# Optimization experiments

Measured on AMD Instinct MI355X. Metric: run time of the kernel, lower is better.

Reference implementation:

```python
import jax, jax.numpy as jnp
import numpy as np

NUM_HEADS = 12
HEAD_DIM = 64
HIDDEN = NUM_HEADS * HEAD_DIM  # 768


def setup_inputs() -> dict:
    key = jax.random.key(0)
    ks = jax.random.split(key, 18)
    B, Ni, Nt, H = 8, 1024, 512, HIDDEN
    inp = {
        "hidden_states": jax.random.normal(ks[0], (B, Ni, H), jnp.float32),
        "text": jax.random.normal(ks[1], (B, Nt, H), jnp.float32),
    }
    names = ["Wq", "Wk", "Wv", "Wqt", "Wkt", "Wvt", "Wo"]
    for i, n in enumerate(names):
        inp[n] = jax.random.normal(ks[2 + i], (H, H), jnp.float32) * 0.02
        inp["b" + n[1:]] = jnp.zeros((H,), jnp.float32)
    return inp


def _split_heads(x):
    # [B, S, H] -> [B, h, S, dh]
    B, S, _ = x.shape
    return x.reshape(B, S, NUM_HEADS, HEAD_DIM).transpose(0, 2, 1, 3)


def _merge_heads(x):
    # [B, h, S, dh] -> [B, S, H]
    B, h, S, dh = x.shape
    return x.transpose(0, 2, 1, 3).reshape(B, S, h * dh)


def _attend(q, k, v):
    scale = 1.0 / jnp.sqrt(jnp.asarray(HEAD_DIM, q.dtype))
    scores = jnp.einsum("bhqd,bhkd->bhqk", q, k) * scale
    probs = jax.nn.softmax(scores, axis=-1)
    ctx = jnp.einsum("bhqk,bhkd->bhqd", probs, v)
    return ctx, probs


def reference(hidden_states, text, Wq, bq, Wk, bk, Wv, bv,
              Wqt, bqt, Wkt, bkt, Wvt, bvt, Wo, bo):
    q_i = _split_heads(hidden_states @ Wq + bq)
    k_i = _split_heads(hidden_states @ Wk + bk)
    v_i = _split_heads(hidden_states @ Wv + bv)
    q_t = _split_heads(text @ Wqt + bqt)
    k_t = _split_heads(text @ Wkt + bkt)
    v_t = _split_heads(text @ Wvt + bvt)

    ctx_ii, weights = _attend(q_i, k_i, v_i)   # img -> img (weights returned, vis=True)
    ctx_tt, _ = _attend(q_t, k_t, v_t)         # text -> text
    ctx_it, _ = _attend(q_i, k_t, v_t)         # img queries, text keys/values
    ctx_ti, _ = _attend(q_t, k_i, v_i)         # text queries, img keys/values

    out_img = (_merge_heads(ctx_ii) + _merge_heads(ctx_it)) * 0.5 @ Wo + bo
    out_text = (_merge_heads(ctx_tt) + _merge_heads(ctx_ti)) * 0.5 @ Wo + bo
    return out_img, out_text, weights
```

## Files before the change

### kernel.cpp

```cpp
#include <hip/hip_runtime.h>

typedef __attribute__((ext_vector_type(4))) float f32x4;
typedef __attribute__((ext_vector_type(8))) short short8;
typedef __attribute__((ext_vector_type(4))) short s16x4;
typedef __attribute__((ext_vector_type(4))) unsigned short us4;
typedef unsigned short u16;
typedef unsigned char uchar;

__device__ __forceinline__ u16 f2b(float f) {
  union { float f; unsigned u; } a; a.f = f;
  unsigned r = a.u + 0x7fffu + ((a.u >> 16) & 1u);
  return (u16)(r >> 16);
}
__device__ __forceinline__ unsigned cvtpk2(float lo, float hi) {
  unsigned r;
  asm("v_cvt_pk_bf16_f32 %0, %1, %2" : "=v"(r) : "v"(lo), "v"(hi));
  return r;
}
__device__ __forceinline__ short8 cvt8(f32x4 a, f32x4 b) {
  union { unsigned u[4]; short8 s; } r;
  r.u[0] = cvtpk2(a[0], a[1]); r.u[1] = cvtpk2(a[2], a[3]);
  r.u[2] = cvtpk2(b[0], b[1]); r.u[3] = cvtpk2(b[2], b[3]);
  return r.s;
}
#define SWZ(r, byteoff) ((((r) * 128) + (byteoff)) ^ (((r) & 7) << 4))
#define C2 0.18033688011112158f

typedef __attribute__((address_space(1))) const void* gp1;
typedef __attribute__((address_space(3))) void* lp3;
__device__ __forceinline__ void gload16(const void* g, void* lds_wave_uniform_base) {
  __builtin_amdgcn_global_load_lds((gp1)g, (lp3)lds_wave_uniform_base, 16, 0, 0);
}
__device__ __forceinline__ void waitv0() { asm volatile("s_waitcnt vmcnt(0)" ::: "memory"); }
__device__ __forceinline__ void waitv1() { asm volatile("s_waitcnt vmcnt(1)" ::: "memory"); }
__device__ __forceinline__ void waitv2() { asm volatile("s_waitcnt vmcnt(2)" ::: "memory"); }
__device__ __forceinline__ void abar()  { __builtin_amdgcn_s_barrier(); }
__device__ __forceinline__ void sbar()  { __builtin_amdgcn_sched_barrier(0); }

__global__ __launch_bounds__(256) void prep_kernel(
    const float* w0, const float* w1, const float* w2, const float* w3,
    const float* w4, const float* w5, const float* w6, u16* wt,
    const float* __restrict__ h, const float* __restrict__ tx, u16* __restrict__ xb)
{
  const int bid = blockIdx.x, t = threadIdx.x;
  if (bid < 1008) {
    __shared__ float tile[64][65];
    const float* Ws[7] = {w0, w1, w2, w3, w4, w5, w6};
    int z = bid / 144, rem = bid % 144;
    const float* W = Ws[z];
    u16* out = wt + (size_t)z * 589824;
    const int r0 = (rem / 12) * 64, c0 = (rem % 12) * 64;
#pragma unroll
    for (int i = 0; i < 4; ++i) {
      int idx = i * 256 + t;
      int r = idx >> 4, c = (idx & 15) * 4;
      f32x4 v = *(const f32x4*)(W + (size_t)(r0 + r) * 768 + (c0 + c));
      tile[r][c + 0] = v[0]; tile[r][c + 1] = v[1];
      tile[r][c + 2] = v[2]; tile[r][c + 3] = v[3];
    }
    __syncthreads();
#pragma unroll
    for (int i = 0; i < 4; ++i) {
      int idx = i * 256 + t;
      int rn = idx >> 4, c = (idx & 15) * 4;
      union { us4 o; unsigned u[2]; } o;
      o.u[0] = cvtpk2(tile[c + 0][rn], tile[c + 1][rn]);
      o.u[1] = cvtpk2(tile[c + 2][rn], tile[c + 3][rn]);
      *(us4*)(out + (size_t)(c0 + rn) * 768 + (r0 + c)) = o.o;
    }
  } else {
    size_t e = ((size_t)(bid - 1008) * 256 + t) * 8;
    const float* src; size_t off;
    if (e < 6291456) { src = h; off = e; } else { src = tx; off = e - 6291456; }
    f32x4 v0 = *(const f32x4*)(src + off), v1 = *(const f32x4*)(src + off + 4);
    *(short8*)(xb + e) = cvt8(v0, v1);
  }
}

__global__ __launch_bounds__(256) void proj_kernel(
    const u16* __restrict__ Xb, const u16* __restrict__ wt,
    const float* __restrict__ bq, const float* __restrict__ bk, const float* __restrict__ bv,
    const float* __restrict__ bqt, const float* __restrict__ bkt, const float* __restrict__ bvt,
    u16* __restrict__ qi, u16* __restrict__ ki, u16* __restrict__ vti,
    u16* __restrict__ qt, u16* __restrict__ ktx, u16* __restrict__ vtt)
{
  const int bid = blockIdx.x;
  const int wk = (bid & 7) * 216 + (bid >> 3);
  const bool img = wk < 1152;
  const int id = img ? wk : wk - 1152;
  const int sg = id / 72, r72 = id % 72;
  const int y = r72 >> 2;
  const int x = sg * 4 + (r72 & 3);
  const int z = y / 6, n0 = (y % 6) * 128, m0 = x * 128;
  const int S = img ? 1024 : 512, logS = img ? 10 : 9;
  const u16* X = img ? Xb : Xb + 6291456;
  const u16* Wt = wt + (img ? 0 : (size_t)3 * 589824) + (size_t)y * 98304;
  const float* bias = img ? (z == 0 ? bq : z == 1 ? bk : bv)
                          : (z == 0 ? bqt : z == 1 ? bkt : bvt);
  u16* out = img ? (z == 0 ? qi : z == 1 ? ki : vti)
                 : (z == 0 ? qt : z == 1 ? ktx : vtt);
  const bool vmode = (z == 2);
  __shared__ unsigned char sm[36864];
  unsigned char* Asm = sm;
  unsigned char* Bsm = sm + 16384;
  const int t = threadIdx.x, w = t >> 6, l = t & 63;
  const int wm = (w & 1) * 64, wn = (w >> 1) * 64;
  f32x4 acc[4][4] = {};
  for (int k0 = 0; k0 < 768; k0 += 64) {
#pragma unroll
    for (int j = 0; j < 4; ++j) {
      int chunk = j * 4 + w;
      int r = chunk * 8 + (l >> 3);
      int cb = ((l & 7) * 16) ^ ((r & 7) << 4);
      gload16(X + (size_t)(m0 + r) * 768 + k0 + cb / 2, Asm + chunk * 1024);
    }
#pragma unroll
    for (int j = 0; j < 4; ++j) {
      int chunk = j * 4 + w;
      int r = chunk * 8 + (l >> 3);
      int cb = ((l & 7) * 16) ^ ((r & 7) << 4);
      gload16(Wt + (size_t)r * 768 + k0 + cb / 2, Bsm + chunk * 1024);
    }
    __syncthreads();
#pragma unroll
    for (int kc = 0; kc < 2; ++kc) {
      short8 af[4], bfr[4];
      const int koff = (kc * 32 + (l >> 4) * 8) * 2;
#pragma unroll
      for (int ms = 0; ms < 4; ++ms) {
        int row = wm + ms * 16 + (l & 15);
        af[ms] = *(const short8*)(Asm + SWZ(row, koff));
      }
#pragma unroll
      for (int ns = 0; ns < 4; ++ns) {
        int row = wn + ns * 16 + (l & 15);
        bfr[ns] = *(const short8*)(Bsm + SWZ(row, koff));
      }
      __builtin_amdgcn_s_setprio(1);
#pragma unroll
      for (int ms = 0; ms < 4; ++ms)
#pragma unroll
        for (int ns = 0; ns < 4; ++ns)
          acc[ms][ns] = __builtin_amdgcn_mfma_f32_16x16x32_bf16(af[ms], bfr[ns], acc[ms][ns], 0, 0, 0);
      __builtin_amdgcn_s_setprio(0);
    }
    __syncthreads();
  }
  float bvv[4];
#pragma unroll
  for (int ns = 0; ns < 4; ++ns) bvv[ns] = bias[n0 + wn + ns * 16 + (l & 15)];
#pragma unroll
  for (int ms = 0; ms < 4; ++ms)
#pragma unroll
    for (int ns = 0; ns < 4; ++ns)
#pragma unroll
      for (int i = 0; i < 4; ++i) {
        u16 u = f2b(acc[ms][ns][i] + bvv[ns]);
        int mm = wm + ms * 16 + (l >> 4) * 4 + i;
        int nn = wn + ns * 16 + (l & 15);
        int row = vmode ? nn : mm, col = vmode ? mm : nn;
        *(u16*)(sm + row * 272 + col * 2) = u;
      }
  __syncthreads();
  if (!vmode) {
#pragma unroll
    for (int i = 0; i < 8; ++i) {
      int idx = i * 256 + t;
      int r = idx >> 4, c = (idx & 15) * 8;
      short8 v = *(const short8*)(sm + r * 272 + c * 2);
      int sg2 = m0 + r, b = sg2 >> logS, s = sg2 & (S - 1);
      int n = n0 + c, hh = n >> 6, d = n & 63;
      *(short8*)(out + (((size_t)b * 12 + hh) * S + s) * 64 + d) = v;
    }
  } else {
#pragma unroll
    for (int i = 0; i < 8; ++i) {
      int idx = i * 256 + t;
      int r = idx >> 4, c = (idx & 15) * 8;
      short8 v = *(const short8*)(sm + r * 272 + c * 2);
      int n = n0 + r, hh = n >> 6, d = n & 63;
      int sg2 = m0 + c, b = sg2 >> logS, s = sg2 & (S - 1);
      *(short8*)(out + (((size_t)b * 12 + hh) * 64 + d) * S + s) = v;
    }
  }
}

__device__ __forceinline__ void stage_k8(const u16* Kp, int kt, uchar* Ksm, int w, int l) {
  int r = w * 8 + (l >> 3);
  int cb = ((l & 7) * 16) ^ ((r & 7) << 4);
  gload16(Kp + (size_t)(kt * 64 + r) * 64 + cb / 2, Ksm + w * 1024);
}
__device__ __forceinline__ void stage_v8(const u16* Vp, int kt, int Sk, uchar* Vsm, int w, int l) {
  int r = w * 8 + (l >> 3);
  int cb = ((l & 7) * 16) ^ ((r & 7) << 4);
  gload16(Vp + (size_t)r * Sk + kt * 64 + cb / 2, Vsm + w * 1024);
}
__device__ __forceinline__ void kfrags(const uchar* Ksm, int l, short8 kf[8]) {
#pragma unroll
  for (int kc = 0; kc < 2; ++kc)
#pragma unroll
    for (int sub = 0; sub < 4; ++sub) {
      int row = sub * 16 + (l & 15);
      kf[kc * 4 + sub] = *(const short8*)(Ksm + SWZ(row, (kc * 32 + (l >> 4) * 8) * 2));
    }
}
__device__ __forceinline__ void qk_swapped(const short8 qf[2], const short8 kf[8], f32x4 sfr[4]) {
  __builtin_amdgcn_s_setprio(1);
#pragma unroll
  for (int kc = 0; kc < 2; ++kc)
#pragma unroll
    for (int sub = 0; sub < 4; ++sub)
      sfr[sub] = __builtin_amdgcn_mfma_f32_16x16x32_bf16(kf[kc * 4 + sub], qf[kc], sfr[sub], 0, 0, 0);
  __builtin_amdgcn_s_setprio(0);
}
__device__ __forceinline__ void vfrags_sigma(const uchar* Vsm, int l, short8 vb[8]) {
#pragma unroll
  for (int kc = 0; kc < 2; ++kc)
#pragma unroll
    for (int ds = 0; ds < 4; ++ds) {
      int row = ds * 16 + (l & 15);
      union { s16x4 h[2]; short8 s; } u;
      u.h[0] = *(const s16x4*)(Vsm + SWZ(row, 64 * kc + 8 * (l >> 4)));
      u.h[1] = *(const s16x4*)(Vsm + SWZ(row, 64 * kc + 32 + 8 * (l >> 4)));
      vb[kc * 4 + ds] = u.s;
    }
}
__device__ __forceinline__ void pa_sigma(const float ps[16], short8 pa[2]) {
#pragma unroll
  for (int kc = 0; kc < 2; ++kc) {
    union { unsigned u[4]; short8 s; } r;
    r.u[0] = cvtpk2(ps[8 * kc + 0], ps[8 * kc + 1]);
    r.u[1] = cvtpk2(ps[8 * kc + 2], ps[8 * kc + 3]);
    r.u[2] = cvtpk2(ps[8 * kc + 4], ps[8 * kc + 5]);
    r.u[3] = cvtpk2(ps[8 * kc + 6], ps[8 * kc + 7]);
    pa[kc] = r.s;
  }
}
__device__ __forceinline__ void pv_sigma(const short8 pa[2], const short8 vb[8], f32x4 og[4]) {
  __builtin_amdgcn_s_setprio(1);
#pragma unroll
  for (int kc = 0; kc < 2; ++kc)
#pragma unroll
    for (int ds = 0; ds < 4; ++ds)
      og[ds] = __builtin_amdgcn_mfma_f32_16x16x32_bf16(pa[kc], vb[kc * 4 + ds], og[ds], 0, 0, 0);
  __builtin_amdgcn_s_setprio(0);
}
__device__ __forceinline__ void pass_unnorm(
    const u16* __restrict__ Kp, const u16* __restrict__ Vp, int Sk,
    const short8 qf[2], uchar* Ks0, uchar* Ks1, uchar* Vs0, uchar* Vs1,
    int w, int l, f32x4 og[4], float& ll)
{
  const int nkt = Sk >> 6;
  stage_k8(Kp, 0, Ks0, w, l);
  stage_v8(Vp, 0, Sk, Vs0, w, l);
  for (int kt = 0; kt < nkt; ++kt) {
    uchar* Kc = (kt & 1) ? Ks1 : Ks0;
    uchar* Vc = (kt & 1) ? Vs1 : Vs0;
    if (kt + 1 < nkt) {
      stage_k8(Kp, kt + 1, (kt & 1) ? Ks0 : Ks1, w, l);
      stage_v8(Vp, kt + 1, Sk, (kt & 1) ? Vs0 : Vs1, w, l);
      waitv2();
    } else {
      waitv0();
    }
    abar(); sbar();
    short8 kf[8];
    kfrags(Kc, l, kf);
    f32x4 sfr[4] = {};
    qk_swapped(qf, kf, sfr);
    float ps[16];
#pragma unroll
    for (int sub = 0; sub < 4; ++sub)
#pragma unroll
      for (int i = 0; i < 4; ++i) {
        float p = exp2f(sfr[sub][i] * C2);
        ll += p;
        ps[sub * 4 + i] = p;
      }
    short8 pa[2];
    pa_sigma(ps, pa);
    short8 vb[8];
    vfrags_sigma(Vc, l, vb);
    pv_sigma(pa, vb, og);
    sbar(); abar();
  }
}

__global__ __launch_bounds__(512, 4) void attn_kernel(
    const u16* __restrict__ qi, const u16* __restrict__ ki, const u16* __restrict__ vti,
    const u16* __restrict__ qt, const u16* __restrict__ ktx, const u16* __restrict__ vtt,
    u16* __restrict__ cimg, u16* __restrict__ ctxt, float* __restrict__ weights)
{
  __shared__ uchar smem[32768];
  const int t = threadIdx.x, w = t >> 6, l = t & 63;
  uchar* Ks0 = smem;
  uchar* Ks1 = smem + 8192;
  uchar* Vs0 = smem + 16384;
  uchar* Vs1 = smem + 24576;

  const int bid = blockIdx.x;
  const int wk = (bid & 7) * 144 + (bid >> 3);
  const bool img = wk < 768;
  const int id = img ? wk : wk - 768;
  const int x = img ? (id & 7) : (id & 3);
  const int head = img ? (id >> 3) : (id >> 2);
  const int b = head / 12, h = head % 12;
  const int Sq = img ? 1024 : 512;
  const int SkA = img ? 1024 : 512, SkB = img ? 512 : 1024;
  const u16* Qp = (img ? qi : qt) + (size_t)head * Sq * 64;
  const u16* KpA = (img ? ki : ktx) + (size_t)head * SkA * 64;
  const u16* VpA = (img ? vti : vtt) + (size_t)head * 64 * SkA;
  const u16* KpB = (img ? ktx : ki) + (size_t)head * SkB * 64;
  const u16* VpB = (img ? vtt : vti) + (size_t)head * 64 * SkB;
  u16* CTX = img ? cimg : ctxt;
  float* PROBS = img ? weights : nullptr;
  const int q0 = x * 128;
  const int qrow = q0 + w * 16 + (l & 15);

  short8 qf[2];
  qf[0] = *(const short8*)(Qp + (size_t)qrow * 64 + (l >> 4) * 8);
  qf[1] = *(const short8*)(Qp + (size_t)qrow * 64 + 32 + (l >> 4) * 8);

  f32x4 of[4] = {};
  if (PROBS) {
    float ll = 0.f;
    const int nkt = SkA >> 6;
    stage_k8(KpA, 0, Ks0, w, l);
    for (int kt = 0; kt < nkt; ++kt) {
      uchar* Kc = (kt & 1) ? Ks1 : Ks0;
      if (kt + 1 < nkt) {
        stage_k8(KpA, kt + 1, (kt & 1) ? Ks0 : Ks1, w, l);
        waitv1();
      } else {
        waitv0();
      }
      abar(); sbar();
      short8 kf[8];
      kfrags(Kc, l, kf);
      f32x4 sfr[4] = {};
      qk_swapped(qf, kf, sfr);
#pragma unroll
      for (int sub = 0; sub < 4; ++sub)
#pragma unroll
        for (int i = 0; i < 4; ++i) ll += exp2f(sfr[sub][i] * C2);
      sbar(); abar();
    }
    stage_k8(KpA, 0, Ks0, w, l);
    stage_v8(VpA, 0, SkA, Vs0, w, l);
    ll += __shfl_xor(ll, 16);
    ll += __shfl_xor(ll, 32);
    const float lb = -__log2f(ll);
    float* prow = PROBS + ((size_t)head * Sq + qrow) * SkA;
    for (int kt = 0; kt < nkt; ++kt) {
      uchar* Kc = (kt & 1) ? Ks1 : Ks0;
      uchar* Vc = (kt & 1) ? Vs1 : Vs0;
      if (kt + 1 < nkt) {
        stage_k8(KpA, kt + 1, (kt & 1) ? Ks0 : Ks1, w, l);
        stage_v8(VpA, kt + 1, SkA, (kt & 1) ? Vs0 : Vs1, w, l);
        waitv2();
      } else {
        waitv0();
      }
      abar(); sbar();
      short8 kf[8];
      kfrags(Kc, l, kf);
      f32x4 sfr[4] = {};
      qk_swapped(qf, kf, sfr);
      float ps[16];
#pragma unroll
      for (int sub = 0; sub < 4; ++sub) {
#pragma unroll
        for (int i = 0; i < 4; ++i)
          ps[sub * 4 + i] = exp2f(sfr[sub][i] * C2 + lb);
        *(f32x4*)(prow + kt * 64 + sub * 16 + (l >> 4) * 4) = *(const f32x4*)&ps[sub * 4];
      }
      short8 pa[2];
      pa_sigma(ps, pa);
      short8 vb[8];
      vfrags_sigma(Vc, l, vb);
      pv_sigma(pa, vb, of);
      sbar(); abar();
    }
#pragma unroll
    for (int ds = 0; ds < 4; ++ds) of[ds] *= 0.5f;
  } else {
    float ll = 0.f;
    pass_unnorm(KpA, VpA, SkA, qf, Ks0, Ks1, Vs0, Vs1, w, l, of, ll);
    ll += __shfl_xor(ll, 16);
    ll += __shfl_xor(ll, 32);
    float r = 0.5f / ll;
#pragma unroll
    for (int i = 0; i < 4; ++i) {
      float lv = __int_as_float(__builtin_amdgcn_ds_bpermute(
          ((l >> 4) * 4 + i) * 4, __float_as_int(r)));
#pragma unroll
      for (int ds = 0; ds < 4; ++ds) of[ds][i] *= lv;
    }
  }
  {
    f32x4 og[4] = {};
    float l2 = 0.f;
    pass_unnorm(KpB, VpB, SkB, qf, Ks0, Ks1, Vs0, Vs1, w, l, og, l2);
    l2 += __shfl_xor(l2, 16);
    l2 += __shfl_xor(l2, 32);
    float r = 0.5f / l2;
#pragma unroll
    for (int i = 0; i < 4; ++i) {
      float lv = __int_as_float(__builtin_amdgcn_ds_bpermute(
          ((l >> 4) * 4 + i) * 4, __float_as_int(r)));
#pragma unroll
      for (int ds = 0; ds < 4; ++ds) of[ds][i] += og[ds][i] * lv;
    }
  }
  __syncthreads();
  {
    uchar* Wb = smem + w * 2176;
#pragma unroll
    for (int ds = 0; ds < 4; ++ds)
#pragma unroll
      for (int i = 0; i < 4; ++i)
        *(u16*)(Wb + ((l >> 4) * 4 + i) * 136 + (16 * ds + (l & 15)) * 2) = f2b(of[ds][i]);
#pragma unroll
    for (int i = 0; i < 2; ++i) {
      int it = i * 64 + l;
      int r = it >> 3, cg = it & 7;
      short8 v = *(const short8*)(Wb + r * 136 + cg * 16);
      int s = q0 + w * 16 + r;
      *(short8*)(CTX + ((size_t)b * Sq + s) * 768 + h * 64 + cg * 8) = v;
    }
  }
}

__global__ __launch_bounds__(256) void outproj_kernel(
    const u16* __restrict__ cimg, const u16* __restrict__ ctxt,
    const u16* __restrict__ Wto, const float* __restrict__ bias,
    float* __restrict__ out_img, float* __restrict__ out_text)
{
  const int bid = blockIdx.x;
  const int wk = (bid & 7) * 72 + (bid >> 3);
  const bool img = wk < 384;
  const int id = img ? wk : wk - 384;
  const int y = img ? (id >> 6) : (id >> 5);
  const int x = img ? (id & 63) : (id & 31);
  const u16* C = img ? cimg : ctxt;
  float* OUT = img ? out_img : out_text;
  const int m0 = x * 128, n0 = y * 128;
  __shared__ unsigned char sm[32768];
  unsigned char* Asm = sm;
  unsigned char* Bsm = sm + 16384;
  const int t = threadIdx.x, w = t >> 6, l = t & 63;
  const int wm = (w & 1) * 64, wn = (w >> 1) * 64;
  f32x4 acc[4][4] = {};
  for (int k0 = 0; k0 < 768; k0 += 64) {
#pragma unroll
    for (int j = 0; j < 4; ++j) {
      int chunk = j * 4 + w;
      int r = chunk * 8 + (l >> 3);
      int cb = ((l & 7) * 16) ^ ((r & 7) << 4);
      gload16(C + (size_t)(m0 + r) * 768 + k0 + cb / 2, Asm + chunk * 1024);
    }
#pragma unroll
    for (int j = 0; j < 4; ++j) {
      int chunk = j * 4 + w;
      int r = chunk * 8 + (l >> 3);
      int cb = ((l & 7) * 16) ^ ((r & 7) << 4);
      gload16(Wto + (size_t)(n0 + r) * 768 + k0 + cb / 2, Bsm + chunk * 1024);
    }
    __syncthreads();
#pragma unroll
    for (int kc = 0; kc < 2; ++kc) {
      short8 af[4], bfr[4];
      const int koff = (kc * 32 + (l >> 4) * 8) * 2;
#pragma unroll
      for (int ms = 0; ms < 4; ++ms) {
        int row = wm + ms * 16 + (l & 15);
        af[ms] = *(const short8*)(Asm + SWZ(row, koff));
      }
#pragma unroll
      for (int ns = 0; ns < 4; ++ns) {
        int row = wn + ns * 16 + (l & 15);
        bfr[ns] = *(const short8*)(Bsm + SWZ(row, koff));
      }
      __builtin_amdgcn_s_setprio(1);
#pragma unroll
      for (int ms = 0; ms < 4; ++ms)
#pragma unroll
        for (int ns = 0; ns < 4; ++ns)
          acc[ms][ns] = __builtin_amdgcn_mfma_f32_16x16x32_bf16(af[ms], bfr[ns], acc[ms][ns], 0, 0, 0);
      __builtin_amdgcn_s_setprio(0);
    }
    __syncthreads();
  }
#pragma unroll
  for (int ms = 0; ms < 4; ++ms)
#pragma unroll
    for (int ns = 0; ns < 4; ++ns) {
      float bv = bias[n0 + wn + ns * 16 + (l & 15)];
#pragma unroll
      for (int i = 0; i < 4; ++i) {
        int mm = m0 + wm + ms * 16 + (l >> 4) * 4 + i;
        int nn = n0 + wn + ns * 16 + (l & 15);
        OUT[(size_t)mm * 768 + nn] = acc[ms][ns][i] + bv;
      }
    }
}

extern "C" void kernel_launch(void* const* d_in, const int* in_sizes, int n_in,
                              void* d_out, int out_size, void* d_ws, size_t ws_size,
                              hipStream_t stream)
{
  const float* hidden = (const float*)d_in[0];
  const float* text   = (const float*)d_in[1];
  const float* Wq  = (const float*)d_in[2];  const float* bq  = (const float*)d_in[3];
  const float* Wk  = (const float*)d_in[4];  const float* bk  = (const float*)d_in[5];
  const float* Wv  = (const float*)d_in[6];  const float* bv  = (const float*)d_in[7];
  const float* Wqt = (const float*)d_in[8];  const float* bqt = (const float*)d_in[9];
  const float* Wkt = (const float*)d_in[10]; const float* bkt = (const float*)d_in[11];
  const float* Wvt = (const float*)d_in[12]; const float* bvt = (const float*)d_in[13];
  const float* Wo  = (const float*)d_in[14]; const float* bo  = (const float*)d_in[15];

  u16* wt   = (u16*)d_ws;
  u16* xb   = wt + 7 * 589824;
  u16* qi   = xb + 9437184;
  u16* ki   = qi + 6291456;
  u16* vti  = ki + 6291456;
  u16* qt   = vti + 6291456;
  u16* ktx  = qt + 3145728;
  u16* vtt  = ktx + 3145728;
  u16* cimg = vtt + 3145728;
  u16* ctxt = cimg + 6291456;

  float* out_img  = (float*)d_out;
  float* out_text = out_img + 6291456;
  float* weights  = out_text + 3145728;

  prep_kernel<<<5616, 256, 0, stream>>>(Wq, Wk, Wv, Wqt, Wkt, Wvt, Wo, wt,
                                        hidden, text, xb);
  proj_kernel<<<1728, 256, 0, stream>>>(xb, wt, bq, bk, bv, bqt, bkt, bvt,
                                        qi, ki, vti, qt, ktx, vtt);
  attn_kernel<<<1152, 512, 0, stream>>>(qi, ki, vti, qt, ktx, vtt,
                                        cimg, ctxt, weights);
  outproj_kernel<<<576, 256, 0, stream>>>(cimg, ctxt, wt + 6 * 589824, bo,
                                          out_img, out_text);
}
```

Before: 313.1 us.

## Triple-buffer K/V tiles in attention and drop the trailing per-iteration barrier

Replaces the double-buffered K/V LDS staging with a three-slot ring and a prefetch distance of two tiles, in both the probability pass and the unnormalized passes. Each loop iteration now issues the next-next tile load after a single barrier, instead of bracketing compute with two barriers. The vmcnt waits are recounted to cover the extra in-flight loads and the probability stores. The aim is more latency hiding and less synchronization, at the cost of LDS growing from 32KB to 48KB per block, which may reduce how many blocks fit on a CU.

```diff
diff --git a/kernel.cpp b/kernel.cpp
--- a/kernel.cpp
+++ b/kernel.cpp
@@ -34,6 +34,8 @@
 __device__ __forceinline__ void waitv0() { asm volatile("s_waitcnt vmcnt(0)" ::: "memory"); }
 __device__ __forceinline__ void waitv1() { asm volatile("s_waitcnt vmcnt(1)" ::: "memory"); }
 __device__ __forceinline__ void waitv2() { asm volatile("s_waitcnt vmcnt(2)" ::: "memory"); }
+__device__ __forceinline__ void waitv4() { asm volatile("s_waitcnt vmcnt(4)" ::: "memory"); }
+__device__ __forceinline__ void waitv6() { asm volatile("s_waitcnt vmcnt(6)" ::: "memory"); }
 __device__ __forceinline__ void abar()  { __builtin_amdgcn_s_barrier(); }
 __device__ __forceinline__ void sbar()  { __builtin_amdgcn_sched_barrier(0); }
 
@@ -247,23 +249,24 @@
 }
 __device__ __forceinline__ void pass_unnorm(
     const u16* __restrict__ Kp, const u16* __restrict__ Vp, int Sk,
-    const short8 qf[2], uchar* Ks0, uchar* Ks1, uchar* Vs0, uchar* Vs1,
-    int w, int l, f32x4 og[4], float& ll)
+    const short8 qf[2], uchar* smem, int w, int l, f32x4 og[4], float& ll)
 {
   const int nkt = Sk >> 6;
-  stage_k8(Kp, 0, Ks0, w, l);
-  stage_v8(Vp, 0, Sk, Vs0, w, l);
+  stage_k8(Kp, 0, smem, w, l);
+  stage_v8(Vp, 0, Sk, smem + 24576, w, l);
+  stage_k8(Kp, 1, smem + 8192, w, l);
+  stage_v8(Vp, 1, Sk, smem + 24576 + 8192, w, l);
   for (int kt = 0; kt < nkt; ++kt) {
-    uchar* Kc = (kt & 1) ? Ks1 : Ks0;
-    uchar* Vc = (kt & 1) ? Vs1 : Vs0;
-    if (kt + 1 < nkt) {
-      stage_k8(Kp, kt + 1, (kt & 1) ? Ks0 : Ks1, w, l);
-      stage_v8(Vp, kt + 1, Sk, (kt & 1) ? Vs0 : Vs1, w, l);
-      waitv2();
-    } else {
-      waitv0();
-    }
+    if (kt + 1 < nkt) waitv2(); else waitv0();
     abar(); sbar();
+    if (kt + 2 < nkt) {
+      int bi = (kt + 2) % 3;
+      stage_k8(Kp, kt + 2, smem + bi * 8192, w, l);
+      stage_v8(Vp, kt + 2, Sk, smem + 24576 + bi * 8192, w, l);
+    }
+    int ci = kt % 3;
+    const uchar* Kc = smem + ci * 8192;
+    const uchar* Vc = smem + 24576 + ci * 8192;
     short8 kf[8];
     kfrags(Kc, l, kf);
     f32x4 sfr[4] = {};
@@ -282,8 +285,9 @@
     short8 vb[8];
     vfrags_sigma(Vc, l, vb);
     pv_sigma(pa, vb, og);
-    sbar(); abar();
-  }
+    sbar();
+  }
+  abar();
 }
 
 __global__ __launch_bounds__(512, 4) void attn_kernel(
@@ -291,12 +295,8 @@
     const u16* __restrict__ qt, const u16* __restrict__ ktx, const u16* __restrict__ vtt,
     u16* __restrict__ cimg, u16* __restrict__ ctxt, float* __restrict__ weights)
 {
-  __shared__ uchar smem[32768];
+  __shared__ uchar smem[49152];
   const int t = threadIdx.x, w = t >> 6, l = t & 63;
-  uchar* Ks0 = smem;
-  uchar* Ks1 = smem + 8192;
-  uchar* Vs0 = smem + 16384;
-  uchar* Vs1 = smem + 24576;
 
   const int bid = blockIdx.x;
   const int wk = (bid & 7) * 144 + (bid >> 3);
@@ -325,43 +325,45 @@
   if (PROBS) {
     float ll = 0.f;
     const int nkt = SkA >> 6;
-    stage_k8(KpA, 0, Ks0, w, l);
+    stage_k8(KpA, 0, smem, w, l);
+    stage_k8(KpA, 1, smem + 8192, w, l);
     for (int kt = 0; kt < nkt; ++kt) {
-      uchar* Kc = (kt & 1) ? Ks1 : Ks0;
-      if (kt + 1 < nkt) {
-        stage_k8(KpA, kt + 1, (kt & 1) ? Ks0 : Ks1, w, l);
-        waitv1();
-      } else {
-        waitv0();
-      }
+      if (kt + 1 < nkt) waitv1(); else waitv0();
       abar(); sbar();
+      if (kt + 2 < nkt)
+        stage_k8(KpA, kt + 2, smem + ((kt + 2) % 3) * 8192, w, l);
       short8 kf[8];
-      kfrags(Kc, l, kf);
+      kfrags(smem + (kt % 3) * 8192, l, kf);
       f32x4 sfr[4] = {};
       qk_swapped(qf, kf, sfr);
 #pragma unroll
       for (int sub = 0; sub < 4; ++sub)
 #pragma unroll
         for (int i = 0; i < 4; ++i) ll += exp2f(sfr[sub][i] * C2);
-      sbar(); abar();
-    }
-    stage_k8(KpA, 0, Ks0, w, l);
-    stage_v8(VpA, 0, SkA, Vs0, w, l);
+      sbar();
+    }
+    abar();
+    stage_k8(KpA, 0, smem, w, l);
+    stage_v8(VpA, 0, SkA, smem + 24576, w, l);
+    stage_k8(KpA, 1, smem + 8192, w, l);
+    stage_v8(VpA, 1, SkA, smem + 24576 + 8192, w, l);
     ll += __shfl_xor(ll, 16);
     ll += __shfl_xor(ll, 32);
     const float lb = -__log2f(ll);
     float* prow = PROBS + ((size_t)head * Sq + qrow) * SkA;
     for (int kt = 0; kt < nkt; ++kt) {
-      uchar* Kc = (kt & 1) ? Ks1 : Ks0;
-      uchar* Vc = (kt & 1) ? Vs1 : Vs0;
-      if (kt + 1 < nkt) {
-        stage_k8(KpA, kt + 1, (kt & 1) ? Ks0 : Ks1, w, l);
-        stage_v8(VpA, kt + 1, SkA, (kt & 1) ? Vs0 : Vs1, w, l);
-        waitv2();
-      } else {
-        waitv0();
-      }
+      if (kt == 0) waitv2();
+      else if (kt + 1 < nkt) waitv6();
+      else waitv4();
       abar(); sbar();
+      if (kt + 2 < nkt) {
+        int bi = (kt + 2) % 3;
+        stage_k8(KpA, kt + 2, smem + bi * 8192, w, l);
+        stage_v8(VpA, kt + 2, SkA, smem + 24576 + bi * 8192, w, l);
+      }
+      int ci = kt % 3;
+      const uchar* Kc = smem + ci * 8192;
+      const uchar* Vc = smem + 24576 + ci * 8192;
       short8 kf[8];
       kfrags(Kc, l, kf);
       f32x4 sfr[4] = {};
@@ -379,13 +381,14 @@
       short8 vb[8];
       vfrags_sigma(Vc, l, vb);
       pv_sigma(pa, vb, of);
-      sbar(); abar();
-    }
+      sbar();
+    }
+    abar();
 #pragma unroll
     for (int ds = 0; ds < 4; ++ds) of[ds] *= 0.5f;
   } else {
     float ll = 0.f;
-    pass_unnorm(KpA, VpA, SkA, qf, Ks0, Ks1, Vs0, Vs1, w, l, of, ll);
+    pass_unnorm(KpA, VpA, SkA, qf, smem, w, l, of, ll);
     ll += __shfl_xor(ll, 16);
     ll += __shfl_xor(ll, 32);
     float r = 0.5f / ll;
@@ -400,7 +403,7 @@
   {
     f32x4 og[4] = {};
     float l2 = 0.f;
-    pass_unnorm(KpB, VpB, SkB, qf, Ks0, Ks1, Vs0, Vs1, w, l, og, l2);
+    pass_unnorm(KpB, VpB, SkB, qf, smem, w, l, og, l2);
     l2 += __shfl_xor(l2, 16);
     l2 += __shfl_xor(l2, 32);
     float r = 0.5f / l2;
```

Result: slower. 326.3 us (+4.2%).
